# Performance work log

Measured on AMD Instinct MI355X. Metric: run time of the kernel, lower is better.

The kernel has to match this reference:

```python
import jax, jax.numpy as jnp
import numpy as np

GAMMA = 10.0    # norm_output gamma for the softmax mask
EPS_BN = 1e-5   # BatchNorm eps
EPS_L2 = 1e-8   # l2norm eps (lavse adds eps to the norm)


def l2norm(x, axis):
    n = jnp.sqrt(jnp.sum(x * x, axis=axis, keepdims=True)) + EPS_L2
    return x / n


def setup_inputs() -> dict:
    key = jax.random.key(0)
    ks = jax.random.split(key, 8)
    Bi, R, D, Bc, T, H = 64, 36, 1024, 32, 64, 128  # H = latent_size // k
    return {
        "img_embed": jax.random.normal(ks[0], (Bi, R, D), jnp.float32),
        "cap_embed": jax.random.normal(ks[1], (Bc, T, D), jnp.float32),
        "Wg1": jax.random.normal(ks[2], (D, H), jnp.float32) * 0.02,
        "bg1": jnp.zeros((H,), jnp.float32),
        "Wg2": jax.random.normal(ks[3], (H, D), jnp.float32) * 0.02,
        "bg2": jnp.zeros((D,), jnp.float32),
        "Wb1": jax.random.normal(ks[4], (D, H), jnp.float32) * 0.02,
        "bb1": jnp.zeros((H,), jnp.float32),
        "Wb2": jax.random.normal(ks[5], (H, D), jnp.float32) * 0.02,
        "bb2": jnp.zeros((D,), jnp.float32),
        "lens": jax.random.randint(ks[6], (Bc,), 4, T - 4, jnp.int32),
    }


def reference(img_embed, cap_embed, Wg1, bg1, Wg2, bg2, Wb1, bb1, Wb2, bb2, lens):
    # cap_embed: (Bc, T, D); ragged mean-pool over the first lens[i] words
    Bc, T, D = cap_embed.shape
    mask = (jnp.arange(T)[None, :] < lens[:, None]).astype(cap_embed.dtype)  # (Bc, T)
    cap_repr = jnp.einsum('btd,bt->bd', cap_embed, mask) / lens[:, None].astype(cap_embed.dtype)

    # img_embed: (Bi, R, D) -> (Bi, D, R); BatchNorm1d (no affine) with batch stats
    x = jnp.transpose(img_embed, (0, 2, 1))
    mean = jnp.mean(x, axis=(0, 2), keepdims=True)          # per-channel over (Bi, R)
    var = jnp.mean((x - mean) ** 2, axis=(0, 2), keepdims=True)
    bn = (x - mean) * jax.lax.rsqrt(var + EPS_BN)           # (Bi, D, R)

    # conditional gamma/beta predicted from each caption vector (1024->128->1024)
    gammas = jax.nn.relu(cap_repr @ Wg1 + bg1) @ Wg2 + bg2  # (Bc, D)
    betas = jax.nn.relu(cap_repr @ Wb1 + bb1) @ Wb2 + bb2   # (Bc, D)

    # vectorized over captions: the torch code loops per caption
    out = bn[None] * gammas[:, None, :, None] + betas[:, None, :, None]  # (Bc, Bi, D, R)
    m = jax.nn.softmax(out * GAMMA, axis=-1)                # softmax mask over regions
    out = m * out

    img_vec = l2norm(jnp.mean(out, axis=-1), -1)            # (Bc, Bi, D)
    cap_vec = l2norm(cap_repr, -1)                          # (Bc, D)
    sims = jnp.einsum('cbd,cd->bc', img_vec, cap_vec)       # (Bi, Bc)
    return sims
```

## Files before the change

### kernel.cpp

```cpp
#include <hip/hip_runtime.h>
#include <math.h>

#define DD 1024
#define HD 128
#define BI 64
#define RR 36
#define BC 32
#define TT 64

#define EPS_BN 1e-5f
#define EPS_L2 1e-8f
#define GAMMA_SM 10.0f
#define LOG2E 1.44269504088896f

#define NBN 64
#define ROWS_BN 36

__global__ __launch_bounds__(256) void k1(const float* __restrict__ cap,
                                          const int* __restrict__ lens,
                                          const float* __restrict__ img,
                                          const float* __restrict__ Wg1,
                                          const float* __restrict__ Wb1,
                                          float* __restrict__ bnpart,
                                          float* __restrict__ repr,
                                          float* __restrict__ sqpart,
                                          float* __restrict__ hp) {
    int bid = blockIdx.x, tid = threadIdx.x;
    if (bid < 512) {
        int e = bid;
        int c = e >> 4, kc = e & 15;
        int len = lens[c];
        __shared__ float4 red[16][17];
        __shared__ float rs[64];
        __shared__ float sqs[16];
        int j = tid & 15, tg = tid >> 4;
        const float4* cp = reinterpret_cast<const float4*>(cap + (size_t)c * TT * DD + kc * 64) + j;
        float4 s = {0.f, 0.f, 0.f, 0.f};
#pragma unroll
        for (int i = 0; i < 4; i++) {
            int t = tg + i * 16;
            if (t < len) {
                float4 x = cp[(size_t)t * 256];
                s.x += x.x; s.y += x.y; s.z += x.z; s.w += x.w;
            }
        }
        red[tg][j] = s;
        __syncthreads();
#pragma unroll
        for (int off = 8; off > 0; off >>= 1) {
            if (tg < off) {
                float4 o = red[tg + off][j];
                red[tg][j].x += o.x; red[tg][j].y += o.y;
                red[tg][j].z += o.z; red[tg][j].w += o.w;
            }
            __syncthreads();
        }
        if (tid < 16) {
            float inv = 1.0f / (float)len;
            float4 v = red[0][tid];
            v.x *= inv; v.y *= inv; v.z *= inv; v.w *= inv;
            rs[tid * 4 + 0] = v.x;
            rs[tid * 4 + 1] = v.y;
            rs[tid * 4 + 2] = v.z;
            rs[tid * 4 + 3] = v.w;
            reinterpret_cast<float4*>(repr)[c * 256 + kc * 16 + tid] = v;
            sqs[tid] = fmaf(v.x, v.x, fmaf(v.y, v.y, fmaf(v.z, v.z, v.w * v.w)));
        }
        __syncthreads();
        if (tid == 0) {
            float s2 = 0.f;
#pragma unroll
            for (int k = 0; k < 16; k++) s2 += sqs[k];
            sqpart[c * 16 + kc] = s2;
        }
        int gb = tid >> 7, h = tid & (HD - 1);
        const float* Wp = (gb ? Wb1 : Wg1) + (size_t)(kc * 64) * HD + h;
        float a0 = 0.f, a1 = 0.f, a2 = 0.f, a3 = 0.f;
#pragma unroll
        for (int d = 0; d < 64; d += 4) {
            a0 = fmaf(rs[d + 0], Wp[(size_t)(d + 0) * HD], a0);
            a1 = fmaf(rs[d + 1], Wp[(size_t)(d + 1) * HD], a1);
            a2 = fmaf(rs[d + 2], Wp[(size_t)(d + 2) * HD], a2);
            a3 = fmaf(rs[d + 3], Wp[(size_t)(d + 3) * HD], a3);
        }
        hp[(size_t)e * 256 + tid] = (a0 + a1) + (a2 + a3);
    } else {
        int g = bid - 512;
        const float4* p = reinterpret_cast<const float4*>(img) + (size_t)g * ROWS_BN * 256 + tid;
        float4 s = {0.f, 0.f, 0.f, 0.f}, q = {0.f, 0.f, 0.f, 0.f};
#pragma unroll
        for (int i = 0; i < ROWS_BN; i++) {
            float4 x = p[(size_t)i * 256];
            s.x += x.x; s.y += x.y; s.z += x.z; s.w += x.w;
            q.x = fmaf(x.x, x.x, q.x); q.y = fmaf(x.y, x.y, q.y);
            q.z = fmaf(x.z, x.z, q.z); q.w = fmaf(x.w, x.w, q.w);
        }
        float4* bp = reinterpret_cast<float4*>(bnpart);
        bp[(g * 2 + 0) * 256 + tid] = s;
        bp[(g * 2 + 1) * 256 + tid] = q;
    }
}

__global__ __launch_bounds__(256) void k2(const float* __restrict__ bnpart,
                                          const float* __restrict__ hp,
                                          const float* __restrict__ bg1,
                                          const float* __restrict__ bb1,
                                          const float* __restrict__ Wg2,
                                          const float* __restrict__ bg2,
                                          const float* __restrict__ Wb2,
                                          const float* __restrict__ bb2,
                                          float* __restrict__ meanp,
                                          float* __restrict__ rstdp,
                                          float* __restrict__ gamma,
                                          float* __restrict__ beta) {
    int bid = blockIdx.x, tid = threadIdx.x;
    __shared__ float lds[512];
    if (bid < 32) {
        int j = bid;
        int dd = tid & 31, gs = tid >> 5;
        int d = j * 32 + dd;
        float s = 0.f, q = 0.f;
#pragma unroll
        for (int g = gs; g < NBN; g += 8) {
            s += bnpart[(size_t)(g * 2 + 0) * DD + d];
            q += bnpart[(size_t)(g * 2 + 1) * DD + d];
        }
        lds[gs * 32 + dd] = s;
        lds[256 + gs * 32 + dd] = q;
        __syncthreads();
        if (gs == 0) {
            float ss = 0.f, qq = 0.f;
#pragma unroll
            for (int k = 0; k < 8; k++) {
                ss += lds[k * 32 + dd];
                qq += lds[256 + k * 32 + dd];
            }
            const float invN = 1.0f / (float)(BI * RR);
            float m = ss * invN;
            float var = fmaf(-m, m, qq * invN);
            meanp[d] = m;
            rstdp[d] = rsqrtf(var + EPS_BN);
        }
    } else {
        int e = bid - 32;
        int c = e >> 3, dg = e & 7;
        int gb = tid >> 7, h = tid & (HD - 1);
        const float* hpp = hp + (size_t)c * 16 * 256 + tid;
        float s = 0.f;
#pragma unroll
        for (int k = 0; k < 16; k++) s += hpp[k * 256];
        lds[tid] = fmaxf(s + (gb ? bb1[h] : bg1[h]), 0.f);
        __syncthreads();
        int d = dg * HD + h;
        const float* Wp = (gb ? Wb2 : Wg2) + d;
        const float* hs = lds + gb * HD;
        float a0 = 0.f, a1 = 0.f, a2 = 0.f, a3 = 0.f;
        float a4 = 0.f, a5 = 0.f, a6 = 0.f, a7 = 0.f;
#pragma unroll
        for (int hh = 0; hh < HD; hh += 8) {
            a0 = fmaf(hs[hh + 0], Wp[(size_t)(hh + 0) * DD], a0);
            a1 = fmaf(hs[hh + 1], Wp[(size_t)(hh + 1) * DD], a1);
            a2 = fmaf(hs[hh + 2], Wp[(size_t)(hh + 2) * DD], a2);
            a3 = fmaf(hs[hh + 3], Wp[(size_t)(hh + 3) * DD], a3);
            a4 = fmaf(hs[hh + 4], Wp[(size_t)(hh + 4) * DD], a4);
            a5 = fmaf(hs[hh + 5], Wp[(size_t)(hh + 5) * DD], a5);
            a6 = fmaf(hs[hh + 6], Wp[(size_t)(hh + 6) * DD], a6);
            a7 = fmaf(hs[hh + 7], Wp[(size_t)(hh + 7) * DD], a7);
        }
        float o = ((a0 + a1) + (a2 + a3)) + ((a4 + a5) + (a6 + a7))
                  + (gb ? bb2[d] : bg2[d]);
        (gb ? beta : gamma)[c * DD + d] = o;
    }
}

__global__ __launch_bounds__(512, 4) void k3(const float* __restrict__ img,
                                             const float* __restrict__ gamma,
                                             const float* __restrict__ beta,
                                             const float* __restrict__ repr,
                                             const float* __restrict__ sqpart,
                                             const float* __restrict__ meanp,
                                             const float* __restrict__ rstdp,
                                             float* __restrict__ sims) {
    int b = blockIdx.x, cg = blockIdx.y;
    int tid = threadIdx.x;
    int lane = tid & 63, wid = tid >> 6;
    __shared__ float invn_l[4];
    if (tid < 64) {
        float v = sqpart[(cg * 4 + (tid >> 4)) * 16 + (tid & 15)];
#pragma unroll
        for (int off = 8; off > 0; off >>= 1) v += __shfl_down(v, off);
        if ((tid & 15) == 0) invn_l[tid >> 4] = 1.0f / (sqrtf(v) + EPS_L2);
    }
    const float2* ip = reinterpret_cast<const float2*>(img + (size_t)b * RR * DD) + tid;
    float2 x[RR];
#pragma unroll
    for (int r = 0; r < RR; r++) x[r] = ip[(size_t)r * 512];
    float2 mn = reinterpret_cast<const float2*>(meanp)[tid];
    float2 rsd = reinterpret_cast<const float2*>(rstdp)[tid];
    __shared__ float sq_l[8][4], dt_l[8][4];
    const float CEXP = GAMMA_SM * LOG2E;
    const float invRC = 1.0f / ((float)RR * CEXP);
    for (int ci = 0; ci < 4; ci++) {
        int c = cg * 4 + ci;
        float2 g  = reinterpret_cast<const float2*>(gamma)[c * 512 + tid];
        float2 bt = reinterpret_cast<const float2*>(beta)[c * 512 + tid];
        float2 cn = reinterpret_cast<const float2*>(repr)[c * 512 + tid];
        float ax = g.x * rsd.x, ay = g.y * rsd.y;
        float apx = ax * CEXP, apy = ay * CEXP;
        float bpx = fmaf(-mn.x, ax, bt.x) * CEXP;
        float bpy = fmaf(-mn.y, ay, bt.y) * CEXP;
        float sex = 0.f, sey = 0.f, sox = 0.f, soy = 0.f;
#pragma unroll
        for (int r = 0; r < RR; r++) {
            float ox = fmaf(apx, x[r].x, bpx);
            float oy = fmaf(apy, x[r].y, bpy);
            float ex_ = exp2f(ox);
            float ey = exp2f(oy);
            sex += ex_; sey += ey;
            sox = fmaf(ex_, ox, sox);
            soy = fmaf(ey, oy, soy);
        }
        float vx = sox / sex * invRC;
        float vy = soy / sey * invRC;
        float sq = fmaf(vx, vx, vy * vy);
        float dt = fmaf(vx, cn.x, vy * cn.y);
#pragma unroll
        for (int off = 32; off > 0; off >>= 1) {
            sq += __shfl_down(sq, off);
            dt += __shfl_down(dt, off);
        }
        if (lane == 0) { sq_l[wid][ci] = sq; dt_l[wid][ci] = dt; }
    }
    __syncthreads();
    if (tid < 4) {
        float sq = 0.f, dt = 0.f;
#pragma unroll
        for (int w = 0; w < 8; w++) { sq += sq_l[w][tid]; dt += dt_l[w][tid]; }
        sims[b * BC + cg * 4 + tid] = dt * invn_l[tid] / (sqrtf(sq) + EPS_L2);
    }
}

extern "C" void kernel_launch(void* const* d_in, const int* in_sizes, int n_in,
                              void* d_out, int out_size, void* d_ws, size_t ws_size,
                              hipStream_t stream) {
    const float* img = (const float*)d_in[0];
    const float* cap = (const float*)d_in[1];
    const float* Wg1 = (const float*)d_in[2];
    const float* bg1 = (const float*)d_in[3];
    const float* Wg2 = (const float*)d_in[4];
    const float* bg2 = (const float*)d_in[5];
    const float* Wb1 = (const float*)d_in[6];
    const float* bb1 = (const float*)d_in[7];
    const float* Wb2 = (const float*)d_in[8];
    const float* bb2 = (const float*)d_in[9];
    const int* lens = (const int*)d_in[10];
    float* out = (float*)d_out;

    float* ws = (float*)d_ws;
    float* bnpart = ws;
    float* repr   = ws + 131072;
    float* sqpart = ws + 163840;
    float* hp     = ws + 164864;
    float* meanp  = ws + 295936;
    float* rstdp  = ws + 296960;
    float* gamma  = ws + 297984;
    float* beta   = ws + 330752;

    k1<<<576, 256, 0, stream>>>(cap, lens, img, Wg1, Wb1, bnpart, repr, sqpart, hp);
    k2<<<288, 256, 0, stream>>>(bnpart, hp, bg1, bb1, Wg2, bg2, Wb2, bb2,
                                meanp, rstdp, gamma, beta);
    k3<<<dim3(BI, 8), 512, 0, stream>>>(img, gamma, beta, repr, sqpart,
                                        meanp, rstdp, out);
}
```

Before: 39.52 us.

## Finish BatchNorm stats in k1 and fold affine coefficients into k2

The BN statistics are now fully reduced inside k1, with each of 64 blocks owning 16 channels across all 2304 rows, so the partial-sum buffer and its second-stage reduction in k2 go away. k2 now also combines gamma/beta with mean/rstd and the softmax scale into precomputed A and B coefficients, which removes per-block recomputation and two loads from k3. The cost is that each BN block reads a narrow 64-byte column strip with a strided loop and a shared-memory tree reduction, which may give worse memory coalescing than the previous row-contiguous partial sums.

Result: slower. 51.51 us (+30.3%).

```diff
diff --git a/kernel.cpp b/kernel.cpp
--- a/kernel.cpp
+++ b/kernel.cpp
@@ -12,19 +12,18 @@
 #define EPS_L2 1e-8f
 #define GAMMA_SM 10.0f
 #define LOG2E 1.44269504088896f
-
-#define NBN 64
-#define ROWS_BN 36
+#define CEXP (GAMMA_SM * LOG2E)
 
 __global__ __launch_bounds__(256) void k1(const float* __restrict__ cap,
                                           const int* __restrict__ lens,
                                           const float* __restrict__ img,
                                           const float* __restrict__ Wg1,
                                           const float* __restrict__ Wb1,
-                                          float* __restrict__ bnpart,
                                           float* __restrict__ repr,
                                           float* __restrict__ sqpart,
-                                          float* __restrict__ hp) {
+                                          float* __restrict__ hp,
+                                          float* __restrict__ meanp,
+                                          float* __restrict__ rstdp) {
     int bid = blockIdx.x, tid = threadIdx.x;
     if (bid < 512) {
         int e = bid;
@@ -85,101 +84,99 @@
         }
         hp[(size_t)e * 256 + tid] = (a0 + a1) + (a2 + a3);
     } else {
-        int g = bid - 512;
-        const float4* p = reinterpret_cast<const float4*>(img) + (size_t)g * ROWS_BN * 256 + tid;
+        int j = bid - 512;
+        int col = tid & 3, rg = tid >> 2;
+        __shared__ float4 ls[256], lq[256];
+        const float4* ip = reinterpret_cast<const float4*>(img) + (size_t)j * 4 + col;
         float4 s = {0.f, 0.f, 0.f, 0.f}, q = {0.f, 0.f, 0.f, 0.f};
-#pragma unroll
-        for (int i = 0; i < ROWS_BN; i++) {
-            float4 x = p[(size_t)i * 256];
+        for (int r = rg; r < BI * RR; r += 64) {
+            float4 x = ip[(size_t)r * 256];
             s.x += x.x; s.y += x.y; s.z += x.z; s.w += x.w;
             q.x = fmaf(x.x, x.x, q.x); q.y = fmaf(x.y, x.y, q.y);
             q.z = fmaf(x.z, x.z, q.z); q.w = fmaf(x.w, x.w, q.w);
         }
-        float4* bp = reinterpret_cast<float4*>(bnpart);
-        bp[(g * 2 + 0) * 256 + tid] = s;
-        bp[(g * 2 + 1) * 256 + tid] = q;
-    }
-}
-
-__global__ __launch_bounds__(256) void k2(const float* __restrict__ bnpart,
-                                          const float* __restrict__ hp,
+        ls[tid] = s; lq[tid] = q;
+        __syncthreads();
+#pragma unroll
+        for (int off = 32; off > 0; off >>= 1) {
+            if (rg < off) {
+                float4 a = ls[tid + off * 4], b = lq[tid + off * 4];
+                ls[tid].x += a.x; ls[tid].y += a.y; ls[tid].z += a.z; ls[tid].w += a.w;
+                lq[tid].x += b.x; lq[tid].y += b.y; lq[tid].z += b.z; lq[tid].w += b.w;
+            }
+            __syncthreads();
+        }
+        if (tid < 4) {
+            const float invN = 1.0f / (float)(BI * RR);
+            float4 ss = ls[tid], qq = lq[tid];
+            float4 m = {ss.x * invN, ss.y * invN, ss.z * invN, ss.w * invN};
+            float4 rs4;
+            rs4.x = rsqrtf(fmaf(-m.x, m.x, qq.x * invN) + EPS_BN);
+            rs4.y = rsqrtf(fmaf(-m.y, m.y, qq.y * invN) + EPS_BN);
+            rs4.z = rsqrtf(fmaf(-m.z, m.z, qq.z * invN) + EPS_BN);
+            rs4.w = rsqrtf(fmaf(-m.w, m.w, qq.w * invN) + EPS_BN);
+            reinterpret_cast<float4*>(meanp)[j * 4 + tid] = m;
+            reinterpret_cast<float4*>(rstdp)[j * 4 + tid] = rs4;
+        }
+    }
+}
+
+__global__ __launch_bounds__(256) void k2(const float* __restrict__ hp,
                                           const float* __restrict__ bg1,
                                           const float* __restrict__ bb1,
                                           const float* __restrict__ Wg2,
                                           const float* __restrict__ bg2,
                                           const float* __restrict__ Wb2,
                                           const float* __restrict__ bb2,
-                                          float* __restrict__ meanp,
-                                          float* __restrict__ rstdp,
-                                          float* __restrict__ gamma,
-                                          float* __restrict__ beta) {
-    int bid = blockIdx.x, tid = threadIdx.x;
-    __shared__ float lds[512];
-    if (bid < 32) {
-        int j = bid;
-        int dd = tid & 31, gs = tid >> 5;
-        int d = j * 32 + dd;
-        float s = 0.f, q = 0.f;
-#pragma unroll
-        for (int g = gs; g < NBN; g += 8) {
-            s += bnpart[(size_t)(g * 2 + 0) * DD + d];
-            q += bnpart[(size_t)(g * 2 + 1) * DD + d];
-        }
-        lds[gs * 32 + dd] = s;
-        lds[256 + gs * 32 + dd] = q;
-        __syncthreads();
-        if (gs == 0) {
-            float ss = 0.f, qq = 0.f;
-#pragma unroll
-            for (int k = 0; k < 8; k++) {
-                ss += lds[k * 32 + dd];
-                qq += lds[256 + k * 32 + dd];
-            }
-            const float invN = 1.0f / (float)(BI * RR);
-            float m = ss * invN;
-            float var = fmaf(-m, m, qq * invN);
-            meanp[d] = m;
-            rstdp[d] = rsqrtf(var + EPS_BN);
-        }
-    } else {
-        int e = bid - 32;
-        int c = e >> 3, dg = e & 7;
-        int gb = tid >> 7, h = tid & (HD - 1);
+                                          const float* __restrict__ meanp,
+                                          const float* __restrict__ rstdp,
+                                          float* __restrict__ Ap,
+                                          float* __restrict__ Bp) {
+    int c = blockIdx.x >> 3, dg = blockIdx.x & 7;
+    int tid = threadIdx.x;
+    int gb = tid >> 7, h = tid & (HD - 1);
+    __shared__ float hid[256];
+    __shared__ float ex[256];
+    {
         const float* hpp = hp + (size_t)c * 16 * 256 + tid;
         float s = 0.f;
 #pragma unroll
         for (int k = 0; k < 16; k++) s += hpp[k * 256];
-        lds[tid] = fmaxf(s + (gb ? bb1[h] : bg1[h]), 0.f);
-        __syncthreads();
-        int d = dg * HD + h;
-        const float* Wp = (gb ? Wb2 : Wg2) + d;
-        const float* hs = lds + gb * HD;
-        float a0 = 0.f, a1 = 0.f, a2 = 0.f, a3 = 0.f;
-        float a4 = 0.f, a5 = 0.f, a6 = 0.f, a7 = 0.f;
-#pragma unroll
-        for (int hh = 0; hh < HD; hh += 8) {
-            a0 = fmaf(hs[hh + 0], Wp[(size_t)(hh + 0) * DD], a0);
-            a1 = fmaf(hs[hh + 1], Wp[(size_t)(hh + 1) * DD], a1);
-            a2 = fmaf(hs[hh + 2], Wp[(size_t)(hh + 2) * DD], a2);
-            a3 = fmaf(hs[hh + 3], Wp[(size_t)(hh + 3) * DD], a3);
-            a4 = fmaf(hs[hh + 4], Wp[(size_t)(hh + 4) * DD], a4);
-            a5 = fmaf(hs[hh + 5], Wp[(size_t)(hh + 5) * DD], a5);
-            a6 = fmaf(hs[hh + 6], Wp[(size_t)(hh + 6) * DD], a6);
-            a7 = fmaf(hs[hh + 7], Wp[(size_t)(hh + 7) * DD], a7);
-        }
-        float o = ((a0 + a1) + (a2 + a3)) + ((a4 + a5) + (a6 + a7))
-                  + (gb ? bb2[d] : bg2[d]);
-        (gb ? beta : gamma)[c * DD + d] = o;
+        hid[tid] = fmaxf(s + (gb ? bb1[h] : bg1[h]), 0.f);
+    }
+    __syncthreads();
+    int d = dg * HD + h;
+    const float* Wp = (gb ? Wb2 : Wg2) + d;
+    const float* hs = hid + gb * HD;
+    float a0 = 0.f, a1 = 0.f, a2 = 0.f, a3 = 0.f;
+    float a4 = 0.f, a5 = 0.f, a6 = 0.f, a7 = 0.f;
+#pragma unroll
+    for (int hh = 0; hh < HD; hh += 8) {
+        a0 = fmaf(hs[hh + 0], Wp[(size_t)(hh + 0) * DD], a0);
+        a1 = fmaf(hs[hh + 1], Wp[(size_t)(hh + 1) * DD], a1);
+        a2 = fmaf(hs[hh + 2], Wp[(size_t)(hh + 2) * DD], a2);
+        a3 = fmaf(hs[hh + 3], Wp[(size_t)(hh + 3) * DD], a3);
+        a4 = fmaf(hs[hh + 4], Wp[(size_t)(hh + 4) * DD], a4);
+        a5 = fmaf(hs[hh + 5], Wp[(size_t)(hh + 5) * DD], a5);
+        a6 = fmaf(hs[hh + 6], Wp[(size_t)(hh + 6) * DD], a6);
+        a7 = fmaf(hs[hh + 7], Wp[(size_t)(hh + 7) * DD], a7);
+    }
+    ex[tid] = ((a0 + a1) + (a2 + a3)) + ((a4 + a5) + (a6 + a7))
+              + (gb ? bb2[d] : bg2[d]);
+    __syncthreads();
+    if (tid < HD) {
+        float a = ex[tid] * rstdp[d];
+        float bv = fmaf(-meanp[d], a, ex[tid + HD]);
+        Ap[c * DD + d] = a * CEXP;
+        Bp[c * DD + d] = bv * CEXP;
     }
 }
 
 __global__ __launch_bounds__(512, 4) void k3(const float* __restrict__ img,
-                                             const float* __restrict__ gamma,
-                                             const float* __restrict__ beta,
+                                             const float* __restrict__ Ap,
+                                             const float* __restrict__ Bp,
                                              const float* __restrict__ repr,
                                              const float* __restrict__ sqpart,
-                                             const float* __restrict__ meanp,
-                                             const float* __restrict__ rstdp,
                                              float* __restrict__ sims) {
     int b = blockIdx.x, cg = blockIdx.y;
     int tid = threadIdx.x;
@@ -195,25 +192,18 @@
     float2 x[RR];
 #pragma unroll
     for (int r = 0; r < RR; r++) x[r] = ip[(size_t)r * 512];
-    float2 mn = reinterpret_cast<const float2*>(meanp)[tid];
-    float2 rsd = reinterpret_cast<const float2*>(rstdp)[tid];
     __shared__ float sq_l[8][4], dt_l[8][4];
-    const float CEXP = GAMMA_SM * LOG2E;
     const float invRC = 1.0f / ((float)RR * CEXP);
     for (int ci = 0; ci < 4; ci++) {
         int c = cg * 4 + ci;
-        float2 g  = reinterpret_cast<const float2*>(gamma)[c * 512 + tid];
-        float2 bt = reinterpret_cast<const float2*>(beta)[c * 512 + tid];
+        float2 ap = reinterpret_cast<const float2*>(Ap)[c * 512 + tid];
+        float2 bp = reinterpret_cast<const float2*>(Bp)[c * 512 + tid];
         float2 cn = reinterpret_cast<const float2*>(repr)[c * 512 + tid];
-        float ax = g.x * rsd.x, ay = g.y * rsd.y;
-        float apx = ax * CEXP, apy = ay * CEXP;
-        float bpx = fmaf(-mn.x, ax, bt.x) * CEXP;
-        float bpy = fmaf(-mn.y, ay, bt.y) * CEXP;
         float sex = 0.f, sey = 0.f, sox = 0.f, soy = 0.f;
 #pragma unroll
         for (int r = 0; r < RR; r++) {
-            float ox = fmaf(apx, x[r].x, bpx);
-            float oy = fmaf(apy, x[r].y, bpy);
+            float ox = fmaf(ap.x, x[r].x, bp.x);
+            float oy = fmaf(ap.y, x[r].y, bp.y);
             float ex_ = exp2f(ox);
             float ey = exp2f(oy);
             sex += ex_; sey += ey;
@@ -257,18 +247,17 @@
     float* out = (float*)d_out;
 
     float* ws = (float*)d_ws;
-    float* bnpart = ws;
-    float* repr   = ws + 131072;
-    float* sqpart = ws + 163840;
-    float* hp     = ws + 164864;
-    float* meanp  = ws + 295936;
-    float* rstdp  = ws + 296960;
-    float* gamma  = ws + 297984;
-    float* beta   = ws + 330752;
-
-    k1<<<576, 256, 0, stream>>>(cap, lens, img, Wg1, Wb1, bnpart, repr, sqpart, hp);
-    k2<<<288, 256, 0, stream>>>(bnpart, hp, bg1, bb1, Wg2, bg2, Wb2, bb2,
-                                meanp, rstdp, gamma, beta);
-    k3<<<dim3(BI, 8), 512, 0, stream>>>(img, gamma, beta, repr, sqpart,
-                                        meanp, rstdp, out);
-}
+    float* repr   = ws;
+    float* sqpart = ws + 32768;
+    float* hp     = ws + 33792;
+    float* meanp  = ws + 164864;
+    float* rstdp  = ws + 165888;
+    float* Ap     = ws + 166912;
+    float* Bp     = ws + 199680;
+
+    k1<<<576, 256, 0, stream>>>(cap, lens, img, Wg1, Wb1,
+                                repr, sqpart, hp, meanp, rstdp);
+    k2<<<256, 256, 0, stream>>>(hp, bg1, bb1, Wg2, bg2, Wb2, bb2,
+                                meanp, rstdp, Ap, Bp);
+    k3<<<dim3(BI, 8), 512, 0, stream>>>(img, Ap, Bp, repr, sqpart, out);
+}
```
